# Kernel tuning notes

Measured on AMD Instinct MI355X. Metric: run time of the kernel, lower is better.

Reference implementation:

```python
import jax, jax.numpy as jnp
import numpy as np
from jax import lax

B, H, OUT, STEPS = 256, 512, 9, 325  # 1 initial step + 325 unrolled steps = 326 outputs


def setup_inputs() -> dict:
    key = jax.random.key(0)
    ks = jax.random.split(key, 12)
    s = 0.05
    return {
        "x": jax.random.normal(ks[0], (B, H), jnp.float32),
        "hx0": jax.random.normal(ks[1], (B, H), jnp.float32),
        "cx0": jax.random.normal(ks[2], (B, H), jnp.float32),
        "W_ih": jax.random.normal(ks[3], (4 * H, H), jnp.float32) * s,
        "W_hh": jax.random.normal(ks[4], (4 * H, H), jnp.float32) * s,
        "b_ih": jax.random.normal(ks[5], (4 * H,), jnp.float32) * s,
        "b_hh": jax.random.normal(ks[6], (4 * H,), jnp.float32) * s,
        "W1": jax.random.normal(ks[7], (H, H), jnp.float32) * s,
        "b1": jax.random.normal(ks[8], (H,), jnp.float32) * s,
        "W2": jax.random.normal(ks[9], (OUT, H), jnp.float32) * s,
        "b2": jax.random.normal(ks[10], (OUT,), jnp.float32) * s,
    }


def reference(x, hx0, cx0, W_ih, W_hh, b_ih, b_hh, W1, b1, W2, b2):
    def lstm_cell(inp, h, c):
        # PyTorch LSTMCell gate order: i, f, g, o
        gates = inp @ W_ih.T + b_ih + h @ W_hh.T + b_hh  # [B, 4H]
        i, f, g, o = jnp.split(gates, 4, axis=-1)
        i = jax.nn.sigmoid(i)
        f = jax.nn.sigmoid(f)
        g = jnp.tanh(g)
        o = jax.nn.sigmoid(o)
        c_new = f * c + i * g
        h_new = o * jnp.tanh(c_new)
        return h_new, c_new

    def mlp(h):
        return jax.nn.relu(h @ W1.T + b1) @ W2.T + b2  # [B, 9]

    h, c = lstm_cell(x, hx0, cx0)
    y0 = mlp(h)

    def step(carry, _):
        h, c = carry
        # original: self.cell(hx, (hx, cx)) -- input IS the current hidden state
        h, c = lstm_cell(h, h, c)
        return (h, c), mlp(h)

    _, ys = lax.scan(step, (h, c), None, length=STEPS)  # ys: [325, B, 9]
    out = jnp.concatenate([y0[None], ys], axis=0)  # [326, B, 9]
    return jnp.transpose(out, (1, 0, 2))  # [B, 326, 9]
```

## Files before the change

kernel.cpp:

```cpp
#include <hip/hip_runtime.h>
#include <cstdio>

#define B_   256
#define H_   512
#define G4_  2048
#define T_   326
#define OUT_ 9

typedef __attribute__((ext_vector_type(8))) short s16x8;
typedef __attribute__((ext_vector_type(4))) float f32x4;
typedef unsigned long long ull;

__device__ inline unsigned short to_bf16(float f) {
    unsigned int u = __builtin_bit_cast(unsigned int, f);
    unsigned int r = (u + 0x7fffu + ((u >> 16) & 1u)) >> 16;
    return (unsigned short)r;
}

__device__ inline float sigmoidf_(float x) { return 1.0f / (1.0f + __expf(-x)); }

__device__ inline float fast_tanh(float x) {
    x = fminf(fmaxf(x, -15.f), 15.f);
    float e = __expf(2.f * x);
    return (e - 1.f) / (e + 1.f);
}


__global__ void prep_weights(const float* __restrict__ Wih, const float* __restrict__ Whh,
                             const float* __restrict__ bih, const float* __restrict__ bhh,
                             unsigned short* __restrict__ Wc, unsigned short* __restrict__ Wcat,
                             float* __restrict__ bc) {
    int idx = blockIdx.x * 256 + threadIdx.x;
    int n = idx >> 9, k = idx & 511;
    float wi = Wih[idx], wh = Whh[idx];
    Wc[idx] = to_bf16(wi + wh);
    Wcat[(n << 10) + k]       = to_bf16(wi);
    Wcat[(n << 10) + 512 + k] = to_bf16(wh);
    if (k == 0) bc[n] = bih[n] + bhh[n];
}

__global__ void prep_w1(const float* __restrict__ W1, unsigned short* __restrict__ W1b) {
    int idx = blockIdx.x * 256 + threadIdx.x;
    W1b[idx] = to_bf16(W1[idx]);
}

__global__ void prep_w2(const float* __restrict__ W2, unsigned short* __restrict__ W2b) {
    int idx = blockIdx.x * 256 + threadIdx.x;
    int o = idx >> 9, k = idx & 511;
    W2b[idx] = (o < OUT_) ? to_bf16(W2[o * H_ + k]) : (unsigned short)0;
}

__global__ void prep_x(const float* __restrict__ x, const float* __restrict__ hx0,
                       unsigned short* __restrict__ xcat) {
    int idx = blockIdx.x * 256 + threadIdx.x;
    int b = idx >> 9, k = idx & 511;
    xcat[(b << 10) + k]       = to_bf16(x[idx]);
    xcat[(b << 10) + 512 + k] = to_bf16(hx0[idx]);
}

template <int KLEN>
__global__ __launch_bounds__(256) void lstm_step(
    const unsigned short* __restrict__ A,
    const unsigned short* __restrict__ W,
    const float* __restrict__ bc,
    const float* __restrict__ c_in,
    float* __restrict__ c_out,
    unsigned short* __restrict__ h_out) {
    const int lane = threadIdx.x & 63;
    const int wave = threadIdx.x >> 6;
    const int mn = lane & 15, q = lane >> 4;
    const int rt = blockIdx.x & 15;
    const int hb = (blockIdx.x >> 4) * 64 + wave * 16;

    const unsigned short* ap  = A + (size_t)(rt * 16 + mn) * KLEN + q * 8;
    const unsigned short* wp0 = W + (size_t)(0 * H_ + hb + mn) * KLEN + q * 8;
    const unsigned short* wp1 = W + (size_t)(1 * H_ + hb + mn) * KLEN + q * 8;
    const unsigned short* wp2 = W + (size_t)(2 * H_ + hb + mn) * KLEN + q * 8;
    const unsigned short* wp3 = W + (size_t)(3 * H_ + hb + mn) * KLEN + q * 8;

    f32x4 acc0 = {0.f,0.f,0.f,0.f}, acc1 = {0.f,0.f,0.f,0.f};
    f32x4 acc2 = {0.f,0.f,0.f,0.f}, acc3 = {0.f,0.f,0.f,0.f};
#pragma unroll 4
    for (int k0 = 0; k0 < KLEN; k0 += 32) {
        s16x8 a  = *reinterpret_cast<const s16x8*>(ap + k0);
        s16x8 w0 = *reinterpret_cast<const s16x8*>(wp0 + k0);
        s16x8 w1 = *reinterpret_cast<const s16x8*>(wp1 + k0);
        s16x8 w2 = *reinterpret_cast<const s16x8*>(wp2 + k0);
        s16x8 w3 = *reinterpret_cast<const s16x8*>(wp3 + k0);
        acc0 = __builtin_amdgcn_mfma_f32_16x16x32_bf16(a, w0, acc0, 0, 0, 0);
        acc1 = __builtin_amdgcn_mfma_f32_16x16x32_bf16(a, w1, acc1, 0, 0, 0);
        acc2 = __builtin_amdgcn_mfma_f32_16x16x32_bf16(a, w2, acc2, 0, 0, 0);
        acc3 = __builtin_amdgcn_mfma_f32_16x16x32_bf16(a, w3, acc3, 0, 0, 0);
    }

    const int j = hb + mn;
    const float bi = bc[j], bfv = bc[H_ + j], bg = bc[2 * H_ + j], bo = bc[3 * H_ + j];
#pragma unroll
    for (int r = 0; r < 4; ++r) {
        const int row = rt * 16 + q * 4 + r;
        const float iv = sigmoidf_(acc0[r] + bi);
        const float fv = sigmoidf_(acc1[r] + bfv);
        const float gv = fast_tanh(acc2[r] + bg);
        const float ov = sigmoidf_(acc3[r] + bo);
        const float co = c_in[row * H_ + j];
        const float cn = fv * co + iv * gv;
        c_out[row * H_ + j] = cn;
        h_out[row * H_ + j] = to_bf16(ov * fast_tanh(cn));
    }
}

__global__ __launch_bounds__(256) void lstm_persist(
    const unsigned short* __restrict__ Wc,
    const float* __restrict__ bc,
    const float* __restrict__ c0,
    unsigned short* __restrict__ h_hist,
    unsigned int* __restrict__ ctr,
    const unsigned short* __restrict__ W1b,
    const float* __restrict__ b1,
    const unsigned short* __restrict__ W2b,
    const float* __restrict__ b2,
    float* __restrict__ out) {
    __shared__ ull smem[4128];
    unsigned short* A_lds = reinterpret_cast<unsigned short*>(smem);
    float* gate_lds = reinterpret_cast<float*>(reinterpret_cast<char*>(smem) + 16384);
    unsigned short* z_lds = reinterpret_cast<unsigned short*>(reinterpret_cast<char*>(smem) + 16384);
    const int tid = threadIdx.x;
    const int lane = tid & 63, wave = tid >> 6;
    const int mn = lane & 15, q = lane >> 4;

    int a_st[8];
#pragma unroll
    for (int p = 0; p < 8; ++p) {
        const int qi = p * 256 + tid;
        const int row = qi >> 7;
        const int bcol = (qi & 127) * 8;
        a_st[p] = row * 512 + ((bcol ^ ((row & 7) << 4)) >> 1);
    }
    int a_rd[16];
#pragma unroll
    for (int kk = 0; kk < 16; ++kk) {
        const int bcol = kk * 64 + q * 16;
        a_rd[kk] = mn * 512 + ((bcol ^ ((mn & 7) << 4)) >> 1);
    }

    if (blockIdx.x < 256) {
        const int g  = blockIdx.x & 15;
        const int jb = (blockIdx.x >> 4) * 32;
        unsigned int* ctr_g = ctr + g * 32;

        s16x8 breg[2][16];
#pragma unroll
        for (int n = 0; n < 2; ++n) {
            const unsigned short* wp = Wc + (size_t)(wave * H_ + jb + n * 16 + mn) * H_ + q * 8;
#pragma unroll
            for (int kk = 0; kk < 16; ++kk)
                breg[n][kk] = *reinterpret_cast<const s16x8*>(wp + kk * 32);
        }
        const float bcv0 = bc[wave * H_ + jb + mn];
        const float bcv1 = bc[wave * H_ + jb + 16 + mn];

        const int crow = tid >> 4, cc0 = (tid & 15) * 2;
        float c_x = c0[(size_t)(g * 16 + crow) * H_ + jb + cc0];
        float c_y = c0[(size_t)(g * 16 + crow) * H_ + jb + cc0 + 1];

        for (int t = 1; t < T_; ++t) {
            const ull* hsrc64 = reinterpret_cast<const ull*>(
                h_hist + (size_t)(t - 1) * (B_ * H_) + (size_t)g * 16 * H_);
            ull vv[8];
#pragma unroll
            for (int p = 0; p < 8; ++p)
                vv[p] = __hip_atomic_load(hsrc64 + p * 256 + tid, __ATOMIC_RELAXED,
                                          __HIP_MEMORY_SCOPE_AGENT);
#pragma unroll
            for (int p = 0; p < 8; ++p)
                *reinterpret_cast<ull*>(&A_lds[a_st[p]]) = vv[p];
            __syncthreads();

            f32x4 acc0 = {0.f,0.f,0.f,0.f}, acc1 = {0.f,0.f,0.f,0.f};
#pragma unroll
            for (int kk = 0; kk < 16; ++kk) {
                s16x8 a = *reinterpret_cast<const s16x8*>(&A_lds[a_rd[kk]]);
                acc0 = __builtin_amdgcn_mfma_f32_16x16x32_bf16(a, breg[0][kk], acc0, 0, 0, 0);
                acc1 = __builtin_amdgcn_mfma_f32_16x16x32_bf16(a, breg[1][kk], acc1, 0, 0, 0);
            }

#pragma unroll
            for (int r = 0; r < 4; ++r) {
                float v0 = acc0[r] + bcv0, v1 = acc1[r] + bcv1;
                if (wave == 2) { v0 = fast_tanh(v0); v1 = fast_tanh(v1); }
                else           { v0 = sigmoidf_(v0); v1 = sigmoidf_(v1); }
                gate_lds[(wave * 16 + (q * 4 + r)) * 33 + mn]      = v0;
                gate_lds[(wave * 16 + (q * 4 + r)) * 33 + 16 + mn] = v1;
            }
            __syncthreads();

            {
                float iv0 = gate_lds[(0 * 16 + crow) * 33 + cc0], iv1 = gate_lds[(0 * 16 + crow) * 33 + cc0 + 1];
                float fv0 = gate_lds[(1 * 16 + crow) * 33 + cc0], fv1 = gate_lds[(1 * 16 + crow) * 33 + cc0 + 1];
                float gv0 = gate_lds[(2 * 16 + crow) * 33 + cc0], gv1 = gate_lds[(2 * 16 + crow) * 33 + cc0 + 1];
                float ov0 = gate_lds[(3 * 16 + crow) * 33 + cc0], ov1 = gate_lds[(3 * 16 + crow) * 33 + cc0 + 1];
                c_x = fv0 * c_x + iv0 * gv0;
                c_y = fv1 * c_y + iv1 * gv1;
                unsigned int h0 = to_bf16(ov0 * fast_tanh(c_x));
                unsigned int h1 = to_bf16(ov1 * fast_tanh(c_y));
                unsigned int packed = h0 | (h1 << 16);
                unsigned int* hdst = reinterpret_cast<unsigned int*>(
                    h_hist + (size_t)t * (B_ * H_) + (size_t)(g * 16 + crow) * H_ + jb + cc0);
                __hip_atomic_store(hdst, packed, __ATOMIC_RELAXED, __HIP_MEMORY_SCOPE_AGENT);
            }

            __syncthreads();
            asm volatile("" ::: "memory");
            if (tid == 0) {
                __hip_atomic_fetch_add(ctr_g, 1u, __ATOMIC_RELAXED, __HIP_MEMORY_SCOPE_AGENT);
                if (t < T_ - 1) {
                    const unsigned int target = 16u * (unsigned int)t;
                    while (__hip_atomic_load(ctr_g, __ATOMIC_RELAXED,
                                             __HIP_MEMORY_SCOPE_AGENT) < target) {
                    }
                }
            }
            asm volatile("" ::: "memory");
            if (t < T_ - 1) __syncthreads();
        }
    } else {
        const int j = blockIdx.x - 256;
        const int xcd = j & 7, mid = j >> 3;

        float b1v[8];
#pragma unroll
        for (int nt = 0; nt < 8; ++nt) b1v[nt] = b1[wave * 128 + nt * 16 + mn];
        const float b2v = (mn < OUT_) ? b2[mn] : 0.f;

        for (int i = mid; i < 2 * T_; i += 16) {
            const int t = i >> 1;
            const int g = xcd + 8 * (i & 1);

            if (tid == 0) {
                const unsigned int tgt = 16u * (unsigned int)t;
                while (__hip_atomic_load(ctr + g * 32, __ATOMIC_RELAXED,
                                         __HIP_MEMORY_SCOPE_AGENT) < tgt)
                    __builtin_amdgcn_s_sleep(4);
            }
            __syncthreads();

            const ull* hsrc64 = reinterpret_cast<const ull*>(
                h_hist + (size_t)t * (B_ * H_) + (size_t)g * 16 * H_);
            ull vv[8];
#pragma unroll
            for (int p = 0; p < 8; ++p)
                vv[p] = __hip_atomic_load(hsrc64 + p * 256 + tid, __ATOMIC_RELAXED,
                                          __HIP_MEMORY_SCOPE_AGENT);
#pragma unroll
            for (int p = 0; p < 8; ++p)
                *reinterpret_cast<ull*>(&A_lds[a_st[p]]) = vv[p];
            __syncthreads();

            f32x4 acc[8];
#pragma unroll
            for (int nt = 0; nt < 8; ++nt) acc[nt] = f32x4{0.f,0.f,0.f,0.f};
            for (int kk = 0; kk < 16; ++kk) {
                s16x8 a = *reinterpret_cast<const s16x8*>(&A_lds[a_rd[kk]]);
#pragma unroll
                for (int nt = 0; nt < 8; ++nt) {
                    s16x8 b = *reinterpret_cast<const s16x8*>(
                        W1b + (size_t)(wave * 128 + nt * 16 + mn) * H_ + kk * 32 + q * 8);
                    acc[nt] = __builtin_amdgcn_mfma_f32_16x16x32_bf16(a, b, acc[nt], 0, 0, 0);
                }
            }
#pragma unroll
            for (int nt = 0; nt < 8; ++nt)
#pragma unroll
                for (int r = 0; r < 4; ++r) {
                    float v = acc[nt][r] + b1v[nt];
                    v = v > 0.f ? v : 0.f;
                    z_lds[(q * 4 + r) * 520 + wave * 128 + nt * 16 + mn] = to_bf16(v);
                }
            __syncthreads();

            if (wave == 0) {
                f32x4 y = {0.f,0.f,0.f,0.f};
#pragma unroll 4
                for (int k0 = 0; k0 < 512; k0 += 32) {
                    s16x8 az = *reinterpret_cast<const s16x8*>(&z_lds[mn * 520 + k0 + q * 8]);
                    s16x8 bw = *reinterpret_cast<const s16x8*>(W2b + (size_t)mn * H_ + k0 + q * 8);
                    y = __builtin_amdgcn_mfma_f32_16x16x32_bf16(az, bw, y, 0, 0, 0);
                }
                if (mn < OUT_) {
#pragma unroll
                    for (int r = 0; r < 4; ++r)
                        out[(size_t)(g * 16 + q * 4 + r) * (T_ * OUT_) + t * OUT_ + mn] = y[r] + b2v;
                }
            }
            __syncthreads();
        }
    }
}

extern "C" void kernel_launch(void* const* d_in, const int* in_sizes, int n_in,
                              void* d_out, int out_size, void* d_ws, size_t ws_size,
                              hipStream_t stream) {
    (void)in_sizes; (void)n_in; (void)out_size;
    const float* x   = (const float*)d_in[0];
    const float* hx0 = (const float*)d_in[1];
    const float* cx0 = (const float*)d_in[2];
    const float* Wih = (const float*)d_in[3];
    const float* Whh = (const float*)d_in[4];
    const float* bih = (const float*)d_in[5];
    const float* bhh = (const float*)d_in[6];
    const float* W1  = (const float*)d_in[7];
    const float* b1  = (const float*)d_in[8];
    const float* W2  = (const float*)d_in[9];
    const float* b2  = (const float*)d_in[10];
    float* out = (float*)d_out;

    char* p = (char*)d_ws;
    size_t off = 0;
    auto alloc = [&](size_t bytes) {
        void* r = p + off;
        off = (off + bytes + 255) & ~(size_t)255;
        return r;
    };
    unsigned short* Wc     = (unsigned short*)alloc((size_t)G4_ * H_ * 2);
    unsigned short* Wcat   = (unsigned short*)alloc((size_t)G4_ * 1024 * 2);
    unsigned short* W1b    = (unsigned short*)alloc((size_t)H_ * H_ * 2);
    unsigned short* W2b    = (unsigned short*)alloc((size_t)16 * H_ * 2);
    float*          bc     = (float*)alloc((size_t)G4_ * 4);
    unsigned short* xcat   = (unsigned short*)alloc((size_t)B_ * 1024 * 2);
    float*          cbuf   = (float*)alloc((size_t)B_ * H_ * 4);
    unsigned int*   ctr    = (unsigned int*)alloc(4096);
    unsigned short* h_hist = (unsigned short*)alloc((size_t)T_ * B_ * H_ * 2);
    if (off > ws_size) {
        fprintf(stderr, "kernel_launch: ws too small: need %zu have %zu\n", off, ws_size);
        return;
    }

    prep_weights<<<G4_ * H_ / 256, 256, 0, stream>>>(Wih, Whh, bih, bhh, Wc, Wcat, bc);
    prep_w1<<<H_ * H_ / 256, 256, 0, stream>>>(W1, W1b);
    prep_w2<<<16 * H_ / 256, 256, 0, stream>>>(W2, W2b);
    prep_x<<<B_ * H_ / 256, 256, 0, stream>>>(x, hx0, xcat);

    lstm_step<1024><<<128, 256, 0, stream>>>(xcat, Wcat, bc, cx0, cbuf, h_hist);

    hipMemsetAsync(ctr, 0, 4096, stream);
    lstm_persist<<<384, 256, 0, stream>>>(Wc, bc, cbuf, h_hist, ctr,
                                          W1b, b1, W2b, b2, out);
}
```

Before: 1.178 ms.

## Halve LSTM recurrence blocks by giving each block 32 batch rows

```diff
diff --git a/kernel.cpp b/kernel.cpp
--- a/kernel.cpp
+++ b/kernel.cpp
@@ -120,9 +120,9 @@
     const unsigned short* __restrict__ W2b,
     const float* __restrict__ b2,
     float* __restrict__ out) {
-    __shared__ ull smem[4128];
+    __shared__ ull smem[6400];
     unsigned short* A_lds = reinterpret_cast<unsigned short*>(smem);
-    float* gate_lds = reinterpret_cast<float*>(reinterpret_cast<char*>(smem) + 16384);
+    float* gate_lds = reinterpret_cast<float*>(reinterpret_cast<char*>(smem) + 32768);
     unsigned short* z_lds = reinterpret_cast<unsigned short*>(reinterpret_cast<char*>(smem) + 16384);
     const int tid = threadIdx.x;
     const int lane = tid & 63, wave = tid >> 6;
@@ -143,9 +143,9 @@
         a_rd[kk] = mn * 512 + ((bcol ^ ((mn & 7) << 4)) >> 1);
     }
 
-    if (blockIdx.x < 256) {
-        const int g  = blockIdx.x & 15;
-        const int jb = (blockIdx.x >> 4) * 32;
+    if (blockIdx.x < 128) {
+        const int g  = blockIdx.x & 7;
+        const int jb = (blockIdx.x >> 3) * 32;
         unsigned int* ctr_g = ctr + g * 32;
 
         s16x8 breg[2][16];
@@ -159,54 +159,78 @@
         const float bcv0 = bc[wave * H_ + jb + mn];
         const float bcv1 = bc[wave * H_ + jb + 16 + mn];
 
-        const int crow = tid >> 4, cc0 = (tid & 15) * 2;
-        float c_x = c0[(size_t)(g * 16 + crow) * H_ + jb + cc0];
-        float c_y = c0[(size_t)(g * 16 + crow) * H_ + jb + cc0 + 1];
+        const int crow = tid >> 3, cc = (tid & 7) * 4;
+        f32x4 creg = *reinterpret_cast<const f32x4*>(&c0[(size_t)(g * 32 + crow) * H_ + jb + cc]);
 
         for (int t = 1; t < T_; ++t) {
             const ull* hsrc64 = reinterpret_cast<const ull*>(
-                h_hist + (size_t)(t - 1) * (B_ * H_) + (size_t)g * 16 * H_);
-            ull vv[8];
-#pragma unroll
-            for (int p = 0; p < 8; ++p)
-                vv[p] = __hip_atomic_load(hsrc64 + p * 256 + tid, __ATOMIC_RELAXED,
-                                          __HIP_MEMORY_SCOPE_AGENT);
-#pragma unroll
-            for (int p = 0; p < 8; ++p)
-                *reinterpret_cast<ull*>(&A_lds[a_st[p]]) = vv[p];
-            __syncthreads();
-
-            f32x4 acc0 = {0.f,0.f,0.f,0.f}, acc1 = {0.f,0.f,0.f,0.f};
+                h_hist + (size_t)(t - 1) * (B_ * H_) + (size_t)g * 32 * H_);
+            {
+                ull vv[8];
+#pragma unroll
+                for (int p = 0; p < 8; ++p)
+                    vv[p] = __hip_atomic_load(hsrc64 + p * 256 + tid, __ATOMIC_RELAXED,
+                                              __HIP_MEMORY_SCOPE_AGENT);
+#pragma unroll
+                for (int p = 0; p < 8; ++p)
+                    *reinterpret_cast<ull*>(&A_lds[a_st[p]]) = vv[p];
+#pragma unroll
+                for (int p = 0; p < 8; ++p)
+                    vv[p] = __hip_atomic_load(hsrc64 + 2048 + p * 256 + tid, __ATOMIC_RELAXED,
+                                              __HIP_MEMORY_SCOPE_AGENT);
+#pragma unroll
+                for (int p = 0; p < 8; ++p)
+                    *reinterpret_cast<ull*>(&A_lds[a_st[p] + 8192]) = vv[p];
+            }
+            __syncthreads();
+
+            f32x4 acc00 = {0.f,0.f,0.f,0.f}, acc01 = {0.f,0.f,0.f,0.f};
+            f32x4 acc10 = {0.f,0.f,0.f,0.f}, acc11 = {0.f,0.f,0.f,0.f};
 #pragma unroll
             for (int kk = 0; kk < 16; ++kk) {
-                s16x8 a = *reinterpret_cast<const s16x8*>(&A_lds[a_rd[kk]]);
-                acc0 = __builtin_amdgcn_mfma_f32_16x16x32_bf16(a, breg[0][kk], acc0, 0, 0, 0);
-                acc1 = __builtin_amdgcn_mfma_f32_16x16x32_bf16(a, breg[1][kk], acc1, 0, 0, 0);
+                s16x8 a0 = *reinterpret_cast<const s16x8*>(&A_lds[a_rd[kk]]);
+                s16x8 a1 = *reinterpret_cast<const s16x8*>(&A_lds[a_rd[kk] + 8192]);
+                acc00 = __builtin_amdgcn_mfma_f32_16x16x32_bf16(a0, breg[0][kk], acc00, 0, 0, 0);
+                acc01 = __builtin_amdgcn_mfma_f32_16x16x32_bf16(a0, breg[1][kk], acc01, 0, 0, 0);
+                acc10 = __builtin_amdgcn_mfma_f32_16x16x32_bf16(a1, breg[0][kk], acc10, 0, 0, 0);
+                acc11 = __builtin_amdgcn_mfma_f32_16x16x32_bf16(a1, breg[1][kk], acc11, 0, 0, 0);
             }
 
 #pragma unroll
             for (int r = 0; r < 4; ++r) {
-                float v0 = acc0[r] + bcv0, v1 = acc1[r] + bcv1;
-                if (wave == 2) { v0 = fast_tanh(v0); v1 = fast_tanh(v1); }
-                else           { v0 = sigmoidf_(v0); v1 = sigmoidf_(v1); }
-                gate_lds[(wave * 16 + (q * 4 + r)) * 33 + mn]      = v0;
-                gate_lds[(wave * 16 + (q * 4 + r)) * 33 + 16 + mn] = v1;
+                float v00 = acc00[r] + bcv0, v01 = acc01[r] + bcv1;
+                float v10 = acc10[r] + bcv0, v11 = acc11[r] + bcv1;
+                if (wave == 2) { v00 = fast_tanh(v00); v01 = fast_tanh(v01);
+                                 v10 = fast_tanh(v10); v11 = fast_tanh(v11); }
+                else           { v00 = sigmoidf_(v00); v01 = sigmoidf_(v01);
+                                 v10 = sigmoidf_(v10); v11 = sigmoidf_(v11); }
+                const int r0 = wave * 1152 + (q * 4 + r) * 36;
+                gate_lds[r0 + mn]            = v00;
+                gate_lds[r0 + 16 + mn]       = v01;
+                gate_lds[r0 + 576 + mn]      = v10;
+                gate_lds[r0 + 576 + 16 + mn] = v11;
             }
             __syncthreads();
 
             {
-                float iv0 = gate_lds[(0 * 16 + crow) * 33 + cc0], iv1 = gate_lds[(0 * 16 + crow) * 33 + cc0 + 1];
-                float fv0 = gate_lds[(1 * 16 + crow) * 33 + cc0], fv1 = gate_lds[(1 * 16 + crow) * 33 + cc0 + 1];
-                float gv0 = gate_lds[(2 * 16 + crow) * 33 + cc0], gv1 = gate_lds[(2 * 16 + crow) * 33 + cc0 + 1];
-                float ov0 = gate_lds[(3 * 16 + crow) * 33 + cc0], ov1 = gate_lds[(3 * 16 + crow) * 33 + cc0 + 1];
-                c_x = fv0 * c_x + iv0 * gv0;
-                c_y = fv1 * c_y + iv1 * gv1;
-                unsigned int h0 = to_bf16(ov0 * fast_tanh(c_x));
-                unsigned int h1 = to_bf16(ov1 * fast_tanh(c_y));
-                unsigned int packed = h0 | (h1 << 16);
+                f32x4 iv = *reinterpret_cast<const f32x4*>(&gate_lds[0 * 1152 + crow * 36 + cc]);
+                f32x4 fv = *reinterpret_cast<const f32x4*>(&gate_lds[1 * 1152 + crow * 36 + cc]);
+                f32x4 gv = *reinterpret_cast<const f32x4*>(&gate_lds[2 * 1152 + crow * 36 + cc]);
+                f32x4 ov = *reinterpret_cast<const f32x4*>(&gate_lds[3 * 1152 + crow * 36 + cc]);
+                unsigned int hp[2];
+#pragma unroll
+                for (int jj = 0; jj < 2; ++jj) {
+                    float cn0 = fv[2*jj] * creg[2*jj] + iv[2*jj] * gv[2*jj];
+                    float cn1 = fv[2*jj+1] * creg[2*jj+1] + iv[2*jj+1] * gv[2*jj+1];
+                    creg[2*jj] = cn0; creg[2*jj+1] = cn1;
+                    unsigned int h0 = to_bf16(ov[2*jj] * fast_tanh(cn0));
+                    unsigned int h1 = to_bf16(ov[2*jj+1] * fast_tanh(cn1));
+                    hp[jj] = h0 | (h1 << 16);
+                }
                 unsigned int* hdst = reinterpret_cast<unsigned int*>(
-                    h_hist + (size_t)t * (B_ * H_) + (size_t)(g * 16 + crow) * H_ + jb + cc0);
-                __hip_atomic_store(hdst, packed, __ATOMIC_RELAXED, __HIP_MEMORY_SCOPE_AGENT);
+                    h_hist + (size_t)t * (B_ * H_) + (size_t)(g * 32 + crow) * H_ + jb + cc);
+                __hip_atomic_store(hdst,     hp[0], __ATOMIC_RELAXED, __HIP_MEMORY_SCOPE_AGENT);
+                __hip_atomic_store(hdst + 1, hp[1], __ATOMIC_RELAXED, __HIP_MEMORY_SCOPE_AGENT);
             }
 
             __syncthreads();
@@ -224,7 +248,7 @@
             if (t < T_ - 1) __syncthreads();
         }
     } else {
-        const int j = blockIdx.x - 256;
+        const int j = blockIdx.x - 128;
         const int xcd = j & 7, mid = j >> 3;
 
         float b1v[8];
@@ -234,18 +258,18 @@
 
         for (int i = mid; i < 2 * T_; i += 16) {
             const int t = i >> 1;
-            const int g = xcd + 8 * (i & 1);
+            const int gg = 2 * xcd + (i & 1);
 
             if (tid == 0) {
                 const unsigned int tgt = 16u * (unsigned int)t;
-                while (__hip_atomic_load(ctr + g * 32, __ATOMIC_RELAXED,
+                while (__hip_atomic_load(ctr + xcd * 32, __ATOMIC_RELAXED,
                                          __HIP_MEMORY_SCOPE_AGENT) < tgt)
                     __builtin_amdgcn_s_sleep(4);
             }
             __syncthreads();
 
             const ull* hsrc64 = reinterpret_cast<const ull*>(
-                h_hist + (size_t)t * (B_ * H_) + (size_t)g * 16 * H_);
+                h_hist + (size_t)t * (B_ * H_) + (size_t)gg * 16 * H_);
             ull vv[8];
 #pragma unroll
             for (int p = 0; p < 8; ++p)
@@ -289,7 +313,7 @@
                 if (mn < OUT_) {
 #pragma unroll
                     for (int r = 0; r < 4; ++r)
-                        out[(size_t)(g * 16 + q * 4 + r) * (T_ * OUT_) + t * OUT_ + mn] = y[r] + b2v;
+                        out[(size_t)(gg * 16 + q * 4 + r) * (T_ * OUT_) + t * OUT_ + mn] = y[r] + b2v;
                 }
             }
             __syncthreads();
@@ -343,6 +367,6 @@
     lstm_step<1024><<<128, 256, 0, stream>>>(xcat, Wcat, bc, cx0, cbuf, h_hist);
 
     hipMemsetAsync(ctr, 0, 4096, stream);
-    lstm_persist<<<384, 256, 0, stream>>>(Wc, bc, cbuf, h_hist, ctr,
+    lstm_persist<<<256, 256, 0, stream>>>(Wc, bc, cbuf, h_hist, ctr,
                                           W1b, b1, W2b, b2, out);
 }
```

New measurement: 1.422 ms. 1.21x slower.
